# Performance work log

Measured on AMD Instinct MI355X. Metric: run time of the kernel, lower is better.

The kernel has to match this reference:

```python
import jax, jax.numpy as jnp
import numpy as np

BATCH, N_AGENTS, OBS_DIM, ACTOR_DIM, N_ACTIONS = 8192, 64, 128, 64, 32


def setup_inputs() -> dict:
    key = jax.random.key(0)
    ks = jax.random.split(key, 14)
    s = 0.05
    inp = {
        "O": jax.random.normal(ks[0], (BATCH, N_AGENTS, OBS_DIM), dtype=jnp.float32),
        "W_enc": jax.random.normal(ks[1], (OBS_DIM, ACTOR_DIM), dtype=jnp.float32) * s,
        "b_enc": jax.random.normal(ks[2], (ACTOR_DIM,), dtype=jnp.float32) * s,
        "W1": jax.random.normal(ks[3], (2 * ACTOR_DIM, ACTOR_DIM), dtype=jnp.float32) * s,
        "b1": jax.random.normal(ks[4], (ACTOR_DIM,), dtype=jnp.float32) * s,
        "W2": jax.random.normal(ks[5], (2 * ACTOR_DIM, ACTOR_DIM), dtype=jnp.float32) * s,
        "b2": jax.random.normal(ks[6], (ACTOR_DIM,), dtype=jnp.float32) * s,
        "W3": jax.random.normal(ks[7], (2 * ACTOR_DIM, ACTOR_DIM), dtype=jnp.float32) * s,
        "b3": jax.random.normal(ks[8], (ACTOR_DIM,), dtype=jnp.float32) * s,
        "W4": jax.random.normal(ks[9], (2 * ACTOR_DIM, ACTOR_DIM), dtype=jnp.float32) * s,
        "b4": jax.random.normal(ks[10], (ACTOR_DIM,), dtype=jnp.float32) * s,
        "W_dec": jax.random.normal(ks[11], (N_AGENTS * ACTOR_DIM, N_ACTIONS), dtype=jnp.float32) * s,
        "b_dec": jax.random.normal(ks[12], (N_ACTIONS,), dtype=jnp.float32) * s,
    }
    return inp


def _comm_layer(H, W, b, n_agents):
    # get_commvar: masked mean over other agents, but divided by n_agents
    # (the zeroed self term is included in the mean denominator) ->
    # C_i = (sum_j H_j - H_i) / n_agents, exactly equal to the original math.
    C = (jnp.sum(H, axis=1, keepdims=True) - H) / n_agents  # [B, A, D]
    Hcat = jnp.concatenate([H, C], axis=-1)                 # [B, A, 2D]
    return Hcat @ W + b                                     # no activation (faithful)


def reference(O, W_enc, b_enc, W1, b1, W2, b2, W3, b3, W4, b4, W_dec, b_dec):
    B, A, _ = O.shape
    H = jax.nn.sigmoid(O @ W_enc + b_enc)  # [B, A, D]
    H = _comm_layer(H, W1, b1, A)
    H = _comm_layer(H, W2, b2, A)
    H = _comm_layer(H, W3, b3, A)
    H = _comm_layer(H, W4, b4, A)
    Hf = H.reshape(B, -1)                  # [B, A*D]
    return Hf @ W_dec + b_dec              # [B, n_actions]
```

## Files before the change

### kernel.cpp

```cpp
#include <hip/hip_runtime.h>
#include <stdint.h>


#define BATCHN 8192
#define NAGENT 64
#define OBSD   128
#define DD     64
#define NACT   32

typedef __attribute__((ext_vector_type(8))) short short8;
typedef __attribute__((ext_vector_type(4))) float floatx4;

__device__ __forceinline__ unsigned short f2b(float f) {
    union { float f; uint32_t u; } v; v.f = f;
    uint32_t r = v.u + 0x7FFFu + ((v.u >> 16) & 1u);
    return (unsigned short)(r >> 16);
}

#define OFF_WENC 0
#define OFF_WCAT 16384
#define OFF_WDEC 81920
#define OFF_H4   344064

__global__ __launch_bounds__(256) void prep_kernel(
    const float* __restrict__ Wenc,
    const float* __restrict__ W1, const float* __restrict__ W2,
    const float* __restrict__ W3, const float* __restrict__ W4,
    const float* __restrict__ Wdec,
    unsigned short* __restrict__ ws)
{
    int tid = blockIdx.x * 256 + threadIdx.x;
    if (tid < 8192) {
        int n = tid >> 7, c2 = tid & 127;
        int k = c2 ^ ((n & 7) << 3);
        ws[OFF_WENC/2 + n*128 + c2] = f2b(Wenc[k*64 + n]);
    } else if (tid < 5*8192) {
        int l = (tid - 8192) >> 13;
        int e = (tid - 8192) & 8191;
        int n = e >> 7, c2 = e & 127;
        int k = c2 ^ ((n & 7) << 3);
        const float* W = (l==0) ? W1 : (l==1) ? W2 : (l==2) ? W3 : W4;
        float v = W[k*64 + n];
        if (k < 64) v -= W[(k+64)*64 + n] * (1.0f/64.0f);
        ws[OFF_WCAT/2 + l*8192 + n*128 + c2] = f2b(v);
    } else {
        int e = tid - 5*8192;
        int n = e >> 12, k = e & 4095;
        ws[OFF_WDEC/2 + n*4096 + k] = f2b(Wdec[k*32 + n]);
    }
}

__global__ __launch_bounds__(256, 6) void fused_kernel(
    const float* __restrict__ O,
    const unsigned short* __restrict__ WencT,
    const unsigned short* __restrict__ WcatT,
    const float* __restrict__ b_enc,
    const float* __restrict__ b1, const float* __restrict__ b2,
    const float* __restrict__ b3, const float* __restrict__ b4,
    unsigned short* __restrict__ H4out)
{
    __shared__ __align__(16) unsigned short sW[64*128];
    __shared__ __align__(16) unsigned short sH[64*72];
    __shared__ __align__(16) unsigned short sS[64];
    __shared__ float sPart[4][64];

    const int t = threadIdx.x;
    const int b = blockIdx.x;
    const int lane = t & 63;
    const int w = t >> 6;
    const int m = lane & 15;
    const int q = lane >> 4;
    const int mx = (m & 7) << 3;

    #pragma unroll
    for (int i = 0; i < 4; i++) {
        int c = t + i*256;
        *(uint4*)&sW[c*8] = *(const uint4*)(WencT + c*8);
    }
    __syncthreads();

    floatx4 acc[4];

    #pragma unroll
    for (int nt = 0; nt < 4; nt++) {
        float bias = b_enc[nt*16 + m];
        acc[nt] = (floatx4){bias, bias, bias, bias};
    }
    {
        const float* Ob = O + (size_t)b * (NAGENT*OBSD) + (w*16 + m)*OBSD + q*8;
        #pragma unroll
        for (int s = 0; s < 4; s++) {
            float4 f0 = *(const float4*)(Ob + s*32);
            float4 f1 = *(const float4*)(Ob + s*32 + 4);
            union { short8 s8; unsigned short u[8]; } ua;
            ua.u[0] = f2b(f0.x); ua.u[1] = f2b(f0.y);
            ua.u[2] = f2b(f0.z); ua.u[3] = f2b(f0.w);
            ua.u[4] = f2b(f1.x); ua.u[5] = f2b(f1.y);
            ua.u[6] = f2b(f1.z); ua.u[7] = f2b(f1.w);
            short8 a = ua.s8;
            #pragma unroll
            for (int nt = 0; nt < 4; nt++) {
                short8 bb = *(const short8*)&sW[(nt*16 + m)*128 + ((s*32 + q*8) ^ mx)];
                acc[nt] = __builtin_amdgcn_mfma_f32_16x16x32_bf16(a, bb, acc[nt], 0, 0, 0);
            }
        }
    }
    #pragma unroll
    for (int nt = 0; nt < 4; nt++)
        #pragma unroll
        for (int r = 0; r < 4; r++)
            acc[nt][r] = 1.0f / (1.0f + __expf(-acc[nt][r]));

    #pragma unroll
    for (int nt = 0; nt < 4; nt++) {
        float s = acc[nt][0] + acc[nt][1] + acc[nt][2] + acc[nt][3];
        s += __shfl_xor(s, 16, 64);
        s += __shfl_xor(s, 32, 64);
        if (q == 0) sPart[w][nt*16 + m] = s;
        #pragma unroll
        for (int r = 0; r < 4; r++)
            sH[(w*16 + q*4 + r)*72 + nt*16 + m] = f2b(acc[nt][r]);
    }

    const float* bs[4] = {b1, b2, b3, b4};
    #pragma unroll
    for (int l = 0; l < 4; l++) {
        __syncthreads();
        #pragma unroll
        for (int i = 0; i < 4; i++) {
            int c = t + i*256;
            *(uint4*)&sW[c*8] = *(const uint4*)(WcatT + l*8192 + c*8);
        }
        if (t < 64)
            sS[t] = f2b((sPart[0][t] + sPart[1][t] + sPart[2][t] + sPart[3][t]) * (1.0f/64.0f));
        __syncthreads();

        const float* bl = bs[l];
        #pragma unroll
        for (int nt = 0; nt < 4; nt++) {
            float bias = bl[nt*16 + m];
            acc[nt] = (floatx4){bias, bias, bias, bias};
        }
        #pragma unroll
        for (int s = 0; s < 2; s++) {
            short8 a = *(const short8*)&sH[(w*16 + m)*72 + s*32 + q*8];
            #pragma unroll
            for (int nt = 0; nt < 4; nt++) {
                short8 bb = *(const short8*)&sW[(nt*16 + m)*128 + ((s*32 + q*8) ^ mx)];
                acc[nt] = __builtin_amdgcn_mfma_f32_16x16x32_bf16(a, bb, acc[nt], 0, 0, 0);
            }
        }
        #pragma unroll
        for (int s = 0; s < 2; s++) {
            short8 a = *(const short8*)&sS[s*32 + q*8];
            #pragma unroll
            for (int nt = 0; nt < 4; nt++) {
                short8 bb = *(const short8*)&sW[(nt*16 + m)*128 + (((s+2)*32 + q*8) ^ mx)];
                acc[nt] = __builtin_amdgcn_mfma_f32_16x16x32_bf16(a, bb, acc[nt], 0, 0, 0);
            }
        }

        if (l < 3) {
            #pragma unroll
            for (int nt = 0; nt < 4; nt++) {
                float s = acc[nt][0] + acc[nt][1] + acc[nt][2] + acc[nt][3];
                s += __shfl_xor(s, 16, 64);
                s += __shfl_xor(s, 32, 64);
                if (q == 0) sPart[w][nt*16 + m] = s;
                #pragma unroll
                for (int r = 0; r < 4; r++)
                    sH[(w*16 + q*4 + r)*72 + nt*16 + m] = f2b(acc[nt][r]);
            }
        } else {
            unsigned short* Hb = H4out + (size_t)b * 4096;
            #pragma unroll
            for (int nt = 0; nt < 4; nt++)
                #pragma unroll
                for (int r = 0; r < 4; r++)
                    Hb[(w*16 + q*4 + r)*64 + nt*16 + m] = f2b(acc[nt][r]);
        }
    }
}

__global__ __launch_bounds__(512) void dec_kernel(
    const unsigned short* __restrict__ Hf,
    const unsigned short* __restrict__ WdecT,
    const float* __restrict__ b_dec,
    float* __restrict__ out)
{
    __shared__ float red[8][16][34];
    const int t = threadIdx.x;
    const int wv = t >> 6, lane = t & 63;
    const int m = lane & 15, q = lane >> 4;
    const int rb = blockIdx.x;
    const int kc = wv;

    const unsigned short* aP  = Hf    + (size_t)(rb*16 + m)*4096 + kc*512 + q*8;
    const unsigned short* bP0 = WdecT + (size_t)m*4096        + kc*512 + q*8;
    const unsigned short* bP1 = WdecT + (size_t)(16 + m)*4096 + kc*512 + q*8;

    floatx4 a0 = {0.f, 0.f, 0.f, 0.f}, a1 = {0.f, 0.f, 0.f, 0.f};
    #pragma unroll 4
    for (int s = 0; s < 16; s++) {
        short8 av  = *(const short8*)(aP  + s*32);
        short8 b0v = *(const short8*)(bP0 + s*32);
        short8 b1v = *(const short8*)(bP1 + s*32);
        a0 = __builtin_amdgcn_mfma_f32_16x16x32_bf16(av, b0v, a0, 0, 0, 0);
        a1 = __builtin_amdgcn_mfma_f32_16x16x32_bf16(av, b1v, a1, 0, 0, 0);
    }
    #pragma unroll
    for (int r = 0; r < 4; r++) {
        red[wv][q*4 + r][m]      = a0[r];
        red[wv][q*4 + r][16 + m] = a1[r];
    }
    __syncthreads();
    const int row = t >> 5, col = t & 31;
    float sum = b_dec[col];
    #pragma unroll
    for (int i = 0; i < 8; i++)
        sum += red[i][row][col];
    out[(size_t)(rb*16 + row)*32 + col] = sum;
}

extern "C" void kernel_launch(void* const* d_in, const int* in_sizes, int n_in,
                              void* d_out, int out_size, void* d_ws, size_t ws_size,
                              hipStream_t stream)
{
    const float* O    = (const float*)d_in[0];
    const float* Wenc = (const float*)d_in[1];
    const float* benc = (const float*)d_in[2];
    const float* W1   = (const float*)d_in[3];
    const float* b1   = (const float*)d_in[4];
    const float* W2   = (const float*)d_in[5];
    const float* b2   = (const float*)d_in[6];
    const float* W3   = (const float*)d_in[7];
    const float* b3   = (const float*)d_in[8];
    const float* W4   = (const float*)d_in[9];
    const float* b4   = (const float*)d_in[10];
    const float* Wdec = (const float*)d_in[11];
    const float* bdec = (const float*)d_in[12];
    float* out = (float*)d_out;
    unsigned short* ws = (unsigned short*)d_ws;

    prep_kernel<<<672, 256, 0, stream>>>(Wenc, W1, W2, W3, W4, Wdec, ws);
    fused_kernel<<<BATCHN, 256, 0, stream>>>(O, ws + OFF_WENC/2, ws + OFF_WCAT/2,
                                             benc, b1, b2, b3, b4, ws + OFF_H4/2);
    dec_kernel<<<512, 512, 0, stream>>>(ws + OFF_H4/2, ws + OFF_WDEC/2, bdec, out);
}
```

Measured before the change: 433.8 us.

## Process two samples per block and prefetch next layer weights into registers

Each 512-thread block now handles two batch samples, so the shared weight tiles are loaded once per two samples and the per-block LDS weight staging traffic is halved. The next layer's weights are prefetched into registers before the barrier and written to shared memory at the start of each layer, overlapping global loads with MFMA work. The sigmoid's division is replaced by a hardware reciprocal. Costs are doubled shared buffers for H, partial sums and the mean vector, plus higher register pressure under the new launch bounds.

New measurement: 433.6 us. No clear change (-0.1%).

```diff
diff --git a/kernel.cpp b/kernel.cpp
--- a/kernel.cpp
+++ b/kernel.cpp
@@ -50,7 +50,7 @@
     }
 }
 
-__global__ __launch_bounds__(256, 6) void fused_kernel(
+__global__ __launch_bounds__(512, 8) void fused_kernel(
     const float* __restrict__ O,
     const unsigned short* __restrict__ WencT,
     const unsigned short* __restrict__ WcatT,
@@ -60,21 +60,23 @@
     unsigned short* __restrict__ H4out)
 {
     __shared__ __align__(16) unsigned short sW[64*128];
-    __shared__ __align__(16) unsigned short sH[64*72];
-    __shared__ __align__(16) unsigned short sS[64];
-    __shared__ float sPart[4][64];
+    __shared__ __align__(16) unsigned short sH[2][64*72];
+    __shared__ __align__(16) unsigned short sS[2][64];
+    __shared__ float sPart[2][4][64];
 
     const int t = threadIdx.x;
-    const int b = blockIdx.x;
     const int lane = t & 63;
     const int w = t >> 6;
+    const int h = w >> 2;
+    const int wp = w & 3;
     const int m = lane & 15;
     const int q = lane >> 4;
     const int mx = (m & 7) << 3;
-
-    #pragma unroll
-    for (int i = 0; i < 4; i++) {
-        int c = t + i*256;
+    const int samp = blockIdx.x * 2 + h;
+
+    #pragma unroll
+    for (int i = 0; i < 2; i++) {
+        int c = t + i*512;
         *(uint4*)&sW[c*8] = *(const uint4*)(WencT + c*8);
     }
     __syncthreads();
@@ -87,7 +89,7 @@
         acc[nt] = (floatx4){bias, bias, bias, bias};
     }
     {
-        const float* Ob = O + (size_t)b * (NAGENT*OBSD) + (w*16 + m)*OBSD + q*8;
+        const float* Ob = O + (size_t)samp * (NAGENT*OBSD) + (wp*16 + m)*OBSD + q*8;
         #pragma unroll
         for (int s = 0; s < 4; s++) {
             float4 f0 = *(const float4*)(Ob + s*32);
@@ -105,35 +107,44 @@
             }
         }
     }
+
+    uint4 wr0 = *(const uint4*)(WcatT + t*8);
+    uint4 wr1 = *(const uint4*)(WcatT + (t + 512)*8);
+
     #pragma unroll
     for (int nt = 0; nt < 4; nt++)
         #pragma unroll
         for (int r = 0; r < 4; r++)
-            acc[nt][r] = 1.0f / (1.0f + __expf(-acc[nt][r]));
+            acc[nt][r] = __builtin_amdgcn_rcpf(1.0f + __expf(-acc[nt][r]));
 
     #pragma unroll
     for (int nt = 0; nt < 4; nt++) {
         float s = acc[nt][0] + acc[nt][1] + acc[nt][2] + acc[nt][3];
         s += __shfl_xor(s, 16, 64);
         s += __shfl_xor(s, 32, 64);
-        if (q == 0) sPart[w][nt*16 + m] = s;
+        if (q == 0) sPart[h][wp][nt*16 + m] = s;
         #pragma unroll
         for (int r = 0; r < 4; r++)
-            sH[(w*16 + q*4 + r)*72 + nt*16 + m] = f2b(acc[nt][r]);
+            sH[h][(wp*16 + q*4 + r)*72 + nt*16 + m] = f2b(acc[nt][r]);
     }
 
     const float* bs[4] = {b1, b2, b3, b4};
     #pragma unroll
     for (int l = 0; l < 4; l++) {
         __syncthreads();
-        #pragma unroll
-        for (int i = 0; i < 4; i++) {
-            int c = t + i*256;
-            *(uint4*)&sW[c*8] = *(const uint4*)(WcatT + l*8192 + c*8);
-        }
-        if (t < 64)
-            sS[t] = f2b((sPart[0][t] + sPart[1][t] + sPart[2][t] + sPart[3][t]) * (1.0f/64.0f));
+        *(uint4*)&sW[t*8]         = wr0;
+        *(uint4*)&sW[(t+512)*8]   = wr1;
+        if (t < 128) {
+            int hh = t >> 6, i = t & 63;
+            sS[hh][i] = f2b((sPart[hh][0][i] + sPart[hh][1][i] +
+                             sPart[hh][2][i] + sPart[hh][3][i]) * (1.0f/64.0f));
+        }
         __syncthreads();
+
+        if (l < 3) {
+            wr0 = *(const uint4*)(WcatT + (l+1)*8192 + t*8);
+            wr1 = *(const uint4*)(WcatT + (l+1)*8192 + (t + 512)*8);
+        }
 
         const float* bl = bs[l];
         #pragma unroll
@@ -143,7 +154,7 @@
         }
         #pragma unroll
         for (int s = 0; s < 2; s++) {
-            short8 a = *(const short8*)&sH[(w*16 + m)*72 + s*32 + q*8];
+            short8 a = *(const short8*)&sH[h][(wp*16 + m)*72 + s*32 + q*8];
             #pragma unroll
             for (int nt = 0; nt < 4; nt++) {
                 short8 bb = *(const short8*)&sW[(nt*16 + m)*128 + ((s*32 + q*8) ^ mx)];
@@ -152,7 +163,7 @@
         }
         #pragma unroll
         for (int s = 0; s < 2; s++) {
-            short8 a = *(const short8*)&sS[s*32 + q*8];
+            short8 a = *(const short8*)&sS[h][s*32 + q*8];
             #pragma unroll
             for (int nt = 0; nt < 4; nt++) {
                 short8 bb = *(const short8*)&sW[(nt*16 + m)*128 + (((s+2)*32 + q*8) ^ mx)];
@@ -166,18 +177,18 @@
                 float s = acc[nt][0] + acc[nt][1] + acc[nt][2] + acc[nt][3];
                 s += __shfl_xor(s, 16, 64);
                 s += __shfl_xor(s, 32, 64);
-                if (q == 0) sPart[w][nt*16 + m] = s;
+                if (q == 0) sPart[h][wp][nt*16 + m] = s;
                 #pragma unroll
                 for (int r = 0; r < 4; r++)
-                    sH[(w*16 + q*4 + r)*72 + nt*16 + m] = f2b(acc[nt][r]);
+                    sH[h][(wp*16 + q*4 + r)*72 + nt*16 + m] = f2b(acc[nt][r]);
             }
         } else {
-            unsigned short* Hb = H4out + (size_t)b * 4096;
+            unsigned short* Hb = H4out + (size_t)samp * 4096;
             #pragma unroll
             for (int nt = 0; nt < 4; nt++)
                 #pragma unroll
                 for (int r = 0; r < 4; r++)
-                    Hb[(w*16 + q*4 + r)*64 + nt*16 + m] = f2b(acc[nt][r]);
+                    Hb[(wp*16 + q*4 + r)*64 + nt*16 + m] = f2b(acc[nt][r]);
         }
     }
 }
@@ -243,7 +254,7 @@
     unsigned short* ws = (unsigned short*)d_ws;
 
     prep_kernel<<<672, 256, 0, stream>>>(Wenc, W1, W2, W3, W4, Wdec, ws);
-    fused_kernel<<<BATCHN, 256, 0, stream>>>(O, ws + OFF_WENC/2, ws + OFF_WCAT/2,
-                                             benc, b1, b2, b3, b4, ws + OFF_H4/2);
+    fused_kernel<<<BATCHN/2, 512, 0, stream>>>(O, ws + OFF_WENC/2, ws + OFF_WCAT/2,
+                                               benc, b1, b2, b3, b4, ws + OFF_H4/2);
     dec_kernel<<<512, 512, 0, stream>>>(ws + OFF_H4/2, ws + OFF_WDEC/2, bdec, out);
 }
```
